# Performance work log

Hardware: AMD Instinct MI355X
Metric: run time of the kernel (lower is better)

The kernel has to match this reference:

```python
import jax, jax.numpy as jnp
import numpy as np

N = 100000          # nodes
E = 1_600_000       # edges (before self loops)
F_IN = 128          # node features
H = 4               # heads (gat1)
C = 32              # dim_h
HC = H * C
NC_CLONE = 20 - 1
NC_TYPE = 30 - 1
NEG_SLOPE = 0.2
BN_EPS = 1e-5


def setup_inputs() -> dict:
    key = jax.random.key(0)
    ks = jax.random.split(key, 24)
    rn = lambda k, shape, s=0.1: (jax.random.normal(k, shape, jnp.float32) * s)
    inp = {
        "x": jax.random.normal(ks[0], (N, F_IN), jnp.float32),
        "edge_index": jax.random.randint(ks[1], (2, E), 0, N, jnp.int32),
        "edge_attr": jax.random.uniform(ks[2], (E, 1), jnp.float32),
        # gat1 (GATv2Conv F_IN -> C, heads=H, edge_dim=1)
        "Wl1": rn(ks[3], (F_IN, HC)), "Wr1": rn(ks[4], (F_IN, HC)),
        "We1": rn(ks[5], (1, HC)), "att1": rn(ks[6], (H, C)), "b1": rn(ks[7], (HC,)),
        # skip Linear F_IN -> HC
        "skip_W": rn(ks[8], (F_IN, HC)), "skip_b": rn(ks[9], (HC,)),
        # batchnorm1
        "bn_g": jnp.ones((HC,), jnp.float32), "bn_b": jnp.zeros((HC,), jnp.float32),
        # gat2 (GATv2Conv HC -> C, heads=1, edge_dim=1)
        "Wl2": rn(ks[10], (HC, C)), "Wr2": rn(ks[11], (HC, C)),
        "We2": rn(ks[12], (1, C)), "att2": rn(ks[13], (1, C)), "b2": rn(ks[14], (C,)),
        # heads
        "fc1_W": rn(ks[15], (C, C)), "fc1_b": rn(ks[16], (C,)),
        "Wc": rn(ks[17], (C, NC_CLONE)), "bc": rn(ks[18], (NC_CLONE,)),
        "Wt": rn(ks[19], (C, NC_TYPE)), "bt": rn(ks[20], (NC_TYPE,)),
    }
    return inp


def _add_self_loops(src, dst, eattr, n):
    # PyG add_self_loops with fill_value='mean': loop attr = scatter-mean of edge_attr by dst
    deg = jax.ops.segment_sum(jnp.ones_like(eattr[:, 0]), dst, num_segments=n)
    mean_attr = jax.ops.segment_sum(eattr, dst, num_segments=n) / jnp.clip(deg, 1.0)[:, None]
    loop = jnp.arange(n, dtype=src.dtype)
    return (jnp.concatenate([src, loop]), jnp.concatenate([dst, loop]),
            jnp.concatenate([eattr, mean_attr], axis=0))


def _gatv2(x, src, dst, eattr, Wl, Wr, We, att, bias, heads, ch):
    n = x.shape[0]
    xl = (x @ Wl).reshape(n, heads, ch)   # values & source attention feats
    xr = (x @ Wr).reshape(n, heads, ch)   # target attention feats
    ee = (eattr @ We).reshape(-1, heads, ch)
    m = jax.nn.leaky_relu(xl[src] + xr[dst] + ee, NEG_SLOPE)   # [E,H,C]
    alpha = jnp.einsum('ehc,hc->eh', m, att)                   # [E,H]
    amax = jax.ops.segment_max(alpha, dst, num_segments=n)
    amax = jnp.where(jnp.isfinite(amax), amax, 0.0)
    ex = jnp.exp(alpha - amax[dst])
    den = jax.ops.segment_sum(ex, dst, num_segments=n)
    a = ex / (den[dst] + 1e-16)                                # segment softmax
    out = jax.ops.segment_sum(a[..., None] * xl[src], dst, num_segments=n)
    return out.reshape(n, heads * ch) + bias, a


def reference(x, edge_index, edge_attr, Wl1, Wr1, We1, att1, b1, skip_W, skip_b,
              bn_g, bn_b, Wl2, Wr2, We2, att2, b2, fc1_W, fc1_b, Wc, bc, Wt, bt):
    n = x.shape[0]
    src, dst, ea = _add_self_loops(edge_index[0], edge_index[1], edge_attr, n)
    h, _ = _gatv2(x, src, dst, ea, Wl1, Wr1, We1, att1, b1, H, C)
    h = h + x @ skip_W + skip_b
    mu = jnp.mean(h, axis=0)
    var = jnp.mean(jnp.square(h - mu), axis=0)
    h = (h - mu) * jax.lax.rsqrt(var + BN_EPS) * bn_g + bn_b
    h = jax.nn.elu(h)
    h, w = _gatv2(h, src, dst, ea, Wl2, Wr2, We2, att2, b2, 1, C)
    h = jax.nn.elu(h)
    h_last = jax.nn.relu(h @ fc1_W + fc1_b)
    h_type = jax.nn.log_softmax(h_last @ Wt + bt, axis=1)
    h_clone = jax.nn.log_softmax(h_last @ Wc + bc, axis=1)
    out = jnp.concatenate([h_clone, h_type], axis=1)
    return out, w
```

## Files before the change

### kernel.cpp

```cpp
#include <hip/hip_runtime.h>
#include <math.h>

#define NN 100000
#define EE 1600000
#define FIN 128
#define HCH 128
#define CCH 32
#define NCLONE 19
#define NTYPE 29
#define ETOT (EE + NN)
#define SCAN_B 49
#define LOG2E 1.4426950408889634f

typedef __bf16 bf16_t;
typedef bf16_t bf16x2 __attribute__((ext_vector_type(2)));
typedef bf16_t bf16x4 __attribute__((ext_vector_type(4)));
typedef bf16_t bf16x8 __attribute__((ext_vector_type(8)));
typedef float f32x4 __attribute__((ext_vector_type(4)));

__global__ __launch_bounds__(256) void k_wcvt(const float* __restrict__ Wl1,
                                              const float* __restrict__ Wr1,
                                              const float* __restrict__ Ws,
                                              const float* __restrict__ Wl2,
                                              const float* __restrict__ Wr2,
                                              bf16_t* __restrict__ WbT,
                                              bf16_t* __restrict__ Wb2T) {
    int t = blockIdx.x * 256 + threadIdx.x;
    if (t < 384 * 128) {
        int n = t >> 7, k = t & 127;
        const float* W = (n < 128) ? Wl1 : ((n < 256) ? Wr1 : Ws);
        WbT[t] = (bf16_t)W[k * 128 + (n & 127)];
    } else if (t < 384 * 128 + 64 * 128) {
        int u = t - 384 * 128;
        int n = u >> 7, k = u & 127;
        const float* W = (n < 32) ? Wl2 : Wr2;
        Wb2T[u] = (bf16_t)W[k * 32 + (n & 31)];
    }
}

__global__ __launch_bounds__(256) void k_deg(const int* __restrict__ ei,
                                             int* __restrict__ deg,
                                             int* __restrict__ slot) {
    int e = blockIdx.x * 256 + threadIdx.x;
    if (e < EE) {
        int d = ei[EE + e];
        slot[e] = atomicAdd(&deg[d], 1);
    }
}

__global__ __launch_bounds__(256) void k_scan1(const int* __restrict__ deg,
                                               int* __restrict__ offs,
                                               int* __restrict__ bsum) {
    __shared__ int tsum[256];
    int b = blockIdx.x, tid = threadIdx.x;
    int base = b * 2048;
    int loc[8];
    int s = 0;
    #pragma unroll
    for (int i = 0; i < 8; ++i) {
        int idx = base + tid * 8 + i;
        int d = (idx < NN) ? deg[idx] : 0;
        loc[i] = s; s += d;
    }
    tsum[tid] = s;
    __syncthreads();
    for (int off = 1; off < 256; off <<= 1) {
        int v = (tid >= off) ? tsum[tid - off] : 0;
        __syncthreads();
        tsum[tid] += v;
        __syncthreads();
    }
    int texcl = tsum[tid] - s;
    #pragma unroll
    for (int i = 0; i < 8; ++i) {
        int idx = base + tid * 8 + i;
        if (idx < NN) offs[idx] = texcl + loc[i];
    }
    if (tid == 255) bsum[b] = tsum[255];
}

__global__ void k_scan2(int* __restrict__ bsum) {
    if (threadIdx.x == 0) {
        int run = 0;
        for (int i = 0; i < SCAN_B; ++i) { int t = bsum[i]; bsum[i] = run; run += t; }
    }
}

__global__ __launch_bounds__(256) void k_scan3(int* __restrict__ offs,
                                               const int* __restrict__ bsum) {
    int i = blockIdx.x * 256 + threadIdx.x;
    if (i < NN) offs[i] += bsum[i >> 11];
}

__global__ __launch_bounds__(256) void k_fill(const int* __restrict__ ei,
                                              const float* __restrict__ ea,
                                              const int* __restrict__ offs,
                                              const int* __restrict__ slot,
                                              int2* __restrict__ ep8) {
    int e = blockIdx.x * 256 + threadIdx.x;
    if (e < EE) {
        int d = ei[EE + e];
        int pos = offs[d] + slot[e];
        ep8[pos] = make_int2(ei[e], __float_as_int(ea[e]));
    }
}

__global__ __launch_bounds__(256) void k_gemm1(const float* __restrict__ x,
                                               const bf16_t* __restrict__ WbT,
                                               bf16_t* __restrict__ xl,
                                               bf16_t* __restrict__ xr,
                                               bf16_t* __restrict__ sk) {
    __shared__ bf16_t As[128 * 128];
    __shared__ bf16_t Bs[128 * 128];
    const int tid = threadIdx.x;
    const int row0 = blockIdx.x * 128;
    #pragma unroll
    for (int i = 0; i < 8; ++i) {
        int c = i * 256 + tid;
        int r = c >> 4, g = c & 15;
        int gr = row0 + r;
        bf16x8 v = {};
        if (gr < NN) {
            float4 f0 = *(const float4*)(x + (size_t)gr * 128 + g * 8);
            float4 f1 = *(const float4*)(x + (size_t)gr * 128 + g * 8 + 4);
            v[0] = (bf16_t)f0.x; v[1] = (bf16_t)f0.y; v[2] = (bf16_t)f0.z; v[3] = (bf16_t)f0.w;
            v[4] = (bf16_t)f1.x; v[5] = (bf16_t)f1.y; v[6] = (bf16_t)f1.z; v[7] = (bf16_t)f1.w;
        }
        *(bf16x8*)&As[r * 128 + ((g ^ (r & 7)) * 8)] = v;
    }

    const int wid = tid >> 6, lane = tid & 63;
    const int wm = wid >> 1, wn = wid & 1;
    const int lr = lane & 15, lg = lane >> 4;

    for (int chunk = 0; chunk < 3; ++chunk) {
        const int col0 = chunk * 128;
        bf16_t* __restrict__ out = (chunk == 0) ? xl : ((chunk == 1) ? xr : sk);
        __syncthreads();
        #pragma unroll
        for (int i = 0; i < 8; ++i) {
            int c = i * 256 + tid;
            int n = c >> 4, g = c & 15;
            bf16x8 v = *(const bf16x8*)(WbT + (size_t)(col0 + n) * 128 + g * 8);
            *(bf16x8*)&Bs[n * 128 + ((g ^ (n & 7)) * 8)] = v;
        }
        __syncthreads();

        f32x4 acc[4][4] = {};
        #pragma unroll
        for (int ks = 0; ks < 4; ++ks) {
            int g = ks * 4 + lg;
            bf16x8 b[4];
            #pragma unroll
            for (int ni = 0; ni < 4; ++ni) {
                int n = wn * 64 + ni * 16 + lr;
                b[ni] = *(const bf16x8*)&Bs[n * 128 + ((g ^ (n & 7)) * 8)];
            }
            #pragma unroll
            for (int mi = 0; mi < 4; ++mi) {
                int r = wm * 64 + mi * 16 + lr;
                bf16x8 a = *(const bf16x8*)&As[r * 128 + ((g ^ (r & 7)) * 8)];
                #pragma unroll
                for (int ni = 0; ni < 4; ++ni)
                    acc[mi][ni] = __builtin_amdgcn_mfma_f32_16x16x32_bf16(a, b[ni], acc[mi][ni], 0, 0, 0);
            }
        }
        #pragma unroll
        for (int mi = 0; mi < 4; ++mi)
            #pragma unroll
            for (int ni = 0; ni < 4; ++ni)
                #pragma unroll
                for (int j = 0; j < 4; ++j) {
                    int gr = row0 + wm * 64 + mi * 16 + lg * 4 + j;
                    if (gr >= NN) continue;
                    int n = wn * 64 + ni * 16 + lr;
                    out[(size_t)gr * 128 + n] = (bf16_t)acc[mi][ni][j];
                }
    }
}

__global__ __launch_bounds__(256) void k_gat1(const bf16_t* __restrict__ xl1,
                                              const bf16_t* __restrict__ xr1,
                                              const bf16_t* __restrict__ skb,
                                              const int* __restrict__ offs,
                                              const int* __restrict__ deg,
                                              const int2* __restrict__ ep8,
                                              const float* __restrict__ att1,
                                              const float* __restrict__ we1,
                                              const float* __restrict__ b1,
                                              const float* __restrict__ skipb,
                                              bf16_t* __restrict__ hb,
                                              float* __restrict__ mattr) {
    int v = (blockIdx.x * 256 + threadIdx.x) >> 6;
    if (v >= NN) return;
    int lane = threadIdx.x & 63;
    int sub = lane >> 4;
    int l = lane & 15;
    int c0 = l * 8;
    float at[8], we[8], xr[8];
    {
        float4 t0 = *(const float4*)(att1 + c0);
        float4 t1 = *(const float4*)(att1 + c0 + 4);
        at[0] = t0.x * LOG2E; at[1] = t0.y * LOG2E; at[2] = t0.z * LOG2E; at[3] = t0.w * LOG2E;
        at[4] = t1.x * LOG2E; at[5] = t1.y * LOG2E; at[6] = t1.z * LOG2E; at[7] = t1.w * LOG2E;
        float4 w0 = *(const float4*)(we1 + c0);
        float4 w1 = *(const float4*)(we1 + c0 + 4);
        we[0] = w0.x; we[1] = w0.y; we[2] = w0.z; we[3] = w0.w;
        we[4] = w1.x; we[5] = w1.y; we[6] = w1.z; we[7] = w1.w;
        bf16x8 xrv = *(const bf16x8*)(xr1 + (size_t)v * 128 + c0);
        #pragma unroll
        for (int j = 0; j < 8; ++j) xr[j] = (float)xrv[j];
    }
    float den = 0.f, easum = 0.f;
    float n[8] = {};
    int st = offs[v], dg = deg[v];
    int i = sub;
    int2 e0 = make_int2(0, 0), e1 = make_int2(0, 0), e2 = make_int2(0, 0);
    bf16x8 a0 = {}, a1 = {};
    if (i < dg) e0 = ep8[st + i];
    if (i + 4 < dg) e1 = ep8[st + i + 4];
    if (i + 8 < dg) e2 = ep8[st + i + 8];
    if (i < dg) a0 = *(const bf16x8*)(xl1 + (size_t)e0.x * 128 + c0);
    if (i + 4 < dg) a1 = *(const bf16x8*)(xl1 + (size_t)e1.x * 128 + c0);
    for (; i < dg; i += 4) {
        bf16x8 a2 = {};
        int2 e3 = make_int2(0, 0);
        if (i + 8 < dg) a2 = *(const bf16x8*)(xl1 + (size_t)e2.x * 128 + c0);
        if (i + 12 < dg) e3 = ep8[st + i + 12];
        float ea_ = __int_as_float(e0.y);
        easum += ea_;
        float q = 0.f, xv[8];
        #pragma unroll
        for (int j = 0; j < 8; ++j) {
            xv[j] = (float)a0[j];
            float w_ = xv[j] + fmaf(ea_, we[j], xr[j]);
            w_ = (w_ > 0.f) ? w_ : 0.2f * w_;
            q = fmaf(w_, at[j], q);
        }
        q += __shfl_xor(q, 1, 4);
        q += __shfl_xor(q, 2, 4);
        float ex = exp2f(q);
        den += ex;
        #pragma unroll
        for (int j = 0; j < 8; ++j) n[j] = fmaf(ex, xv[j], n[j]);
        e0 = e1; e1 = e2; e2 = e3; a0 = a1; a1 = a2;
    }
    #pragma unroll
    for (int w_ = 16; w_ <= 32; w_ <<= 1) {
        den += __shfl_xor(den, w_, 64);
        easum += __shfl_xor(easum, w_, 64);
        #pragma unroll
        for (int j = 0; j < 8; ++j) n[j] += __shfl_xor(n[j], w_, 64);
    }
    float eav = easum / fmaxf((float)dg, 1.0f);
    if (lane == 0) mattr[v] = eav;
    bf16x8 svv = *(const bf16x8*)(xl1 + (size_t)v * 128 + c0);
    float qs = 0.f, xs[8];
    #pragma unroll
    for (int j = 0; j < 8; ++j) {
        xs[j] = (float)svv[j];
        float w_ = xs[j] + fmaf(eav, we[j], xr[j]);
        w_ = (w_ > 0.f) ? w_ : 0.2f * w_;
        qs = fmaf(w_, at[j], qs);
    }
    qs += __shfl_xor(qs, 1, 4);
    qs += __shfl_xor(qs, 2, 4);
    {
        float ex = exp2f(qs);
        den += ex;
        #pragma unroll
        for (int j = 0; j < 8; ++j) n[j] = fmaf(ex, xs[j], n[j]);
    }
    if (sub == 0) {
        float inv = 1.0f / (den + 1e-16f);
        float4 bb0 = *(const float4*)(b1 + c0);
        float4 bb1 = *(const float4*)(b1 + c0 + 4);
        float4 sb0 = *(const float4*)(skipb + c0);
        float4 sb1 = *(const float4*)(skipb + c0 + 4);
        bf16x8 skv = *(const bf16x8*)(skb + (size_t)v * 128 + c0);
        float bb[8] = {bb0.x, bb0.y, bb0.z, bb0.w, bb1.x, bb1.y, bb1.z, bb1.w};
        float sv[8] = {sb0.x, sb0.y, sb0.z, sb0.w, sb1.x, sb1.y, sb1.z, sb1.w};
        bf16x8 r;
        #pragma unroll
        for (int j = 0; j < 8; ++j)
            r[j] = (bf16_t)(n[j] * inv + bb[j] + (float)skv[j] + sv[j]);
        *(bf16x8*)(hb + (size_t)v * 128 + c0) = r;
    }
}

__global__ __launch_bounds__(256) void k_bnstats(const bf16_t* __restrict__ h,
                                                 float* __restrict__ bns,
                                                 float* __restrict__ bnq) {
    __shared__ float sS[16 * 128];
    __shared__ float sQ[16 * 128];
    int tid = threadIdx.x;
    int cg = tid & 15;
    int slot = tid >> 4;
    int c0 = cg * 8;
    float s[8] = {}, q[8] = {};
    for (int r = blockIdx.x * 16 + slot; r < NN; r += gridDim.x * 16) {
        bf16x8 v = *(const bf16x8*)&h[(size_t)r * 128 + c0];
        #pragma unroll
        for (int j = 0; j < 8; ++j) { float f = (float)v[j]; s[j] += f; q[j] += f * f; }
    }
    #pragma unroll
    for (int j = 0; j < 8; ++j) { sS[slot * 128 + c0 + j] = s[j]; sQ[slot * 128 + c0 + j] = q[j]; }
    __syncthreads();
    if (tid < 128) {
        float as = 0.f, aq = 0.f;
        #pragma unroll
        for (int k = 0; k < 16; ++k) { as += sS[k * 128 + tid]; aq += sQ[k * 128 + tid]; }
        atomicAdd(&bns[tid], as);
        atomicAdd(&bnq[tid], aq);
    }
}

__global__ void k_bnfinal(const float* __restrict__ bns, const float* __restrict__ bnq,
                          const float* __restrict__ g, const float* __restrict__ b,
                          float* __restrict__ scale, float* __restrict__ shift) {
    int c = threadIdx.x;
    if (c < 128) {
        float mu = bns[c] * (1.0f / NN);
        float var = bnq[c] * (1.0f / NN) - mu * mu;
        float rs = rsqrtf(var + 1e-5f);
        float a = rs * g[c];
        scale[c] = a;
        shift[c] = b[c] - mu * a;
    }
}

__global__ __launch_bounds__(256) void k_gemm2(const bf16_t* __restrict__ h,
                                               const float* __restrict__ scl,
                                               const float* __restrict__ shf,
                                               const bf16_t* __restrict__ Wb2T,
                                               bf16_t* __restrict__ xl2,
                                               float* __restrict__ xr2) {
    __shared__ bf16_t As[128 * 128];
    __shared__ bf16_t Bs[64 * 128];
    const int tid = threadIdx.x;
    const int row0 = blockIdx.x * 128;
    #pragma unroll
    for (int i = 0; i < 8; ++i) {
        int c = i * 256 + tid;
        int r = c >> 4, g = c & 15;
        int gr = row0 + r;
        bf16x8 v = {};
        if (gr < NN) {
            bf16x8 hv = *(const bf16x8*)(h + (size_t)gr * 128 + g * 8);
            float4 s0 = *(const float4*)(scl + g * 8);
            float4 s1 = *(const float4*)(scl + g * 8 + 4);
            float4 t0 = *(const float4*)(shf + g * 8);
            float4 t1 = *(const float4*)(shf + g * 8 + 4);
            float e[8];
            e[0] = (float)hv[0] * s0.x + t0.x; e[1] = (float)hv[1] * s0.y + t0.y;
            e[2] = (float)hv[2] * s0.z + t0.z; e[3] = (float)hv[3] * s0.w + t0.w;
            e[4] = (float)hv[4] * s1.x + t1.x; e[5] = (float)hv[5] * s1.y + t1.y;
            e[6] = (float)hv[6] * s1.z + t1.z; e[7] = (float)hv[7] * s1.w + t1.w;
            #pragma unroll
            for (int j = 0; j < 8; ++j) {
                float vv = e[j];
                vv = (vv > 0.f) ? vv : (__expf(vv) - 1.0f);
                v[j] = (bf16_t)vv;
            }
        }
        *(bf16x8*)&As[r * 128 + ((g ^ (r & 7)) * 8)] = v;
    }
    #pragma unroll
    for (int i = 0; i < 4; ++i) {
        int c = i * 256 + tid;
        int n = c >> 4, g = c & 15;
        bf16x8 v = *(const bf16x8*)(Wb2T + (size_t)n * 128 + g * 8);
        *(bf16x8*)&Bs[n * 128 + ((g ^ (n & 7)) * 8)] = v;
    }
    __syncthreads();

    const int wid = tid >> 6, lane = tid & 63;
    const int wm = wid >> 1, wn = wid & 1;
    const int lr = lane & 15, lg = lane >> 4;
    f32x4 acc[4][2] = {};
    #pragma unroll
    for (int ks = 0; ks < 4; ++ks) {
        int g = ks * 4 + lg;
        bf16x8 b0, b1;
        {
            int n = wn * 32 + lr;
            b0 = *(const bf16x8*)&Bs[n * 128 + ((g ^ (n & 7)) * 8)];
            n += 16;
            b1 = *(const bf16x8*)&Bs[n * 128 + ((g ^ (n & 7)) * 8)];
        }
        #pragma unroll
        for (int mi = 0; mi < 4; ++mi) {
            int r = wm * 64 + mi * 16 + lr;
            bf16x8 a = *(const bf16x8*)&As[r * 128 + ((g ^ (r & 7)) * 8)];
            acc[mi][0] = __builtin_amdgcn_mfma_f32_16x16x32_bf16(a, b0, acc[mi][0], 0, 0, 0);
            acc[mi][1] = __builtin_amdgcn_mfma_f32_16x16x32_bf16(a, b1, acc[mi][1], 0, 0, 0);
        }
    }
    #pragma unroll
    for (int mi = 0; mi < 4; ++mi)
        #pragma unroll
        for (int ni = 0; ni < 2; ++ni)
            #pragma unroll
            for (int j = 0; j < 4; ++j) {
                int gr = row0 + wm * 64 + mi * 16 + lg * 4 + j;
                if (gr >= NN) continue;
                int n = wn * 32 + ni * 16 + lr;
                float val = acc[mi][ni][j];
                if (n < 32) xl2[(size_t)gr * 32 + n] = (bf16_t)val;
                else xr2[(size_t)gr * 32 + (n - 32)] = val;
            }
}

__global__ __launch_bounds__(256) void k_gat2(const bf16_t* __restrict__ xl2,
                                              const float* __restrict__ xr2,
                                              const float* __restrict__ mattr,
                                              const int* __restrict__ offs,
                                              const int* __restrict__ deg,
                                              const int2* __restrict__ ep8,
                                              const float* __restrict__ att2,
                                              const float* __restrict__ we2,
                                              const float* __restrict__ b2,
                                              float* __restrict__ h3,
                                              float* __restrict__ acsr,
                                              float* __restrict__ Inv,
                                              float* __restrict__ wout) {
    int v = (blockIdx.x * 256 + threadIdx.x) >> 6;
    if (v >= NN) return;
    int lane = threadIdx.x & 63;
    int sub = lane >> 3;
    int l = lane & 7;
    int c0 = l * 4;
    float4 atv = *(const float4*)(att2 + c0);
    float4 wev = *(const float4*)(we2 + c0);
    float4 xrv = *(const float4*)(xr2 + (size_t)v * 32 + c0);
    float at[4] = {atv.x * LOG2E, atv.y * LOG2E, atv.z * LOG2E, atv.w * LOG2E};
    float we[4] = {wev.x, wev.y, wev.z, wev.w};
    float xr[4] = {xrv.x, xrv.y, xrv.z, xrv.w};
    float den = 0.f;
    float n[4] = {};
    int st = offs[v], dg = deg[v];
    int i = sub;
    int2 e0 = make_int2(0, 0), e1 = make_int2(0, 0), e2 = make_int2(0, 0);
    bf16x4 a0 = {}, a1 = {};
    if (i < dg) e0 = ep8[st + i];
    if (i + 8 < dg) e1 = ep8[st + i + 8];
    if (i + 16 < dg) e2 = ep8[st + i + 16];
    if (i < dg) a0 = *(const bf16x4*)(xl2 + (size_t)e0.x * 32 + c0);
    if (i + 8 < dg) a1 = *(const bf16x4*)(xl2 + (size_t)e1.x * 32 + c0);
    for (; i < dg; i += 8) {
        bf16x4 a2 = {};
        int2 e3 = make_int2(0, 0);
        if (i + 16 < dg) a2 = *(const bf16x4*)(xl2 + (size_t)e2.x * 32 + c0);
        if (i + 24 < dg) e3 = ep8[st + i + 24];
        float ea_ = __int_as_float(e0.y);
        float q = 0.f, xv[4];
        #pragma unroll
        for (int j = 0; j < 4; ++j) {
            xv[j] = (float)a0[j];
            float w_ = xv[j] + fmaf(ea_, we[j], xr[j]);
            w_ = (w_ > 0.f) ? w_ : 0.2f * w_;
            q = fmaf(w_, at[j], q);
        }
        q += __shfl_xor(q, 1, 8);
        q += __shfl_xor(q, 2, 8);
        q += __shfl_xor(q, 4, 8);
        if (l == 0) acsr[st + i] = q;
        float ex = exp2f(q);
        den += ex;
        #pragma unroll
        for (int j = 0; j < 4; ++j) n[j] = fmaf(ex, xv[j], n[j]);
        e0 = e1; e1 = e2; e2 = e3; a0 = a1; a1 = a2;
    }
    #pragma unroll
    for (int w_ = 8; w_ <= 32; w_ <<= 1) {
        den += __shfl_xor(den, w_, 64);
        #pragma unroll
        for (int j = 0; j < 4; ++j) n[j] += __shfl_xor(n[j], w_, 64);
    }
    float eav = mattr[v];
    bf16x4 sv = *(const bf16x4*)(xl2 + (size_t)v * 32 + c0);
    float qs = 0.f, xs[4];
    #pragma unroll
    for (int j = 0; j < 4; ++j) {
        xs[j] = (float)sv[j];
        float w_ = xs[j] + fmaf(eav, we[j], xr[j]);
        w_ = (w_ > 0.f) ? w_ : 0.2f * w_;
        qs = fmaf(w_, at[j], qs);
    }
    qs += __shfl_xor(qs, 1, 8);
    qs += __shfl_xor(qs, 2, 8);
    qs += __shfl_xor(qs, 4, 8);
    {
        float ex = exp2f(qs);
        den += ex;
        #pragma unroll
        for (int j = 0; j < 4; ++j) n[j] = fmaf(ex, xs[j], n[j]);
    }
    float inv = 1.0f / (den + 1e-16f);
    if (lane == 0) {
        Inv[v] = inv;
        wout[EE + v] = exp2f(qs) * inv;
    }
    if (sub == 0) {
        float4 bb = *(const float4*)(b2 + c0);
        float b_[4] = {bb.x, bb.y, bb.z, bb.w};
        float4 r;
        float* rp = &r.x;
        #pragma unroll
        for (int j = 0; j < 4; ++j) {
            float o = n[j] * inv + b_[j];
            rp[j] = (o > 0.f) ? o : (__expf(o) - 1.0f);
        }
        *(float4*)(h3 + (size_t)v * 32 + c0) = r;
    }
}

__global__ __launch_bounds__(256) void k_wfinal(const int* __restrict__ ei,
                                                const int* __restrict__ offs,
                                                const int* __restrict__ slot,
                                                const float* __restrict__ acsr,
                                                const float* __restrict__ Inv,
                                                float* __restrict__ wout) {
    int e = blockIdx.x * 256 + threadIdx.x;
    if (e >= EE) return;
    int d = ei[EE + e];
    float al = acsr[offs[d] + slot[e]];
    wout[e] = exp2f(al) * Inv[d];
}

__global__ __launch_bounds__(256) void k_head(const float* __restrict__ h3,
                                              const float* __restrict__ fc1W,
                                              const float* __restrict__ fc1b,
                                              const float* __restrict__ Wc,
                                              const float* __restrict__ bc,
                                              const float* __restrict__ Wt,
                                              const float* __restrict__ bt,
                                              float* __restrict__ outp) {
    __shared__ float sW1[32 * 32];
    __shared__ float sWc[32 * NCLONE];
    __shared__ float sWt[32 * NTYPE];
    __shared__ float sb1[32], sbc[NCLONE], sbt[NTYPE];
    int tid = threadIdx.x;
    for (int i = tid; i < 1024; i += 256) sW1[i] = fc1W[i];
    for (int i = tid; i < 32 * NCLONE; i += 256) sWc[i] = Wc[i];
    for (int i = tid; i < 32 * NTYPE; i += 256) sWt[i] = Wt[i];
    if (tid < 32) sb1[tid] = fc1b[tid];
    if (tid < NCLONE) sbc[tid] = bc[tid];
    if (tid < NTYPE) sbt[tid] = bt[tid];
    __syncthreads();
    int g = tid >> 5, l = tid & 31;
    int v = blockIdx.x * 8 + g;
    if (v >= NN) return;
    float x = h3[(size_t)v * CCH + l];
    float acc = sb1[l];
    #pragma unroll
    for (int c = 0; c < 32; ++c) {
        float xc = __shfl(x, c, 32);
        acc += xc * sW1[c * 32 + l];
    }
    float hl = fmaxf(acc, 0.0f);
    float at = (l < NTYPE) ? sbt[l] : 0.0f;
    float ac = (l < NCLONE) ? sbc[l] : 0.0f;
    #pragma unroll
    for (int c = 0; c < 32; ++c) {
        float hc = __shfl(hl, c, 32);
        float wt_ = (l < NTYPE) ? sWt[c * NTYPE + l] : 0.0f;
        float wc_ = (l < NCLONE) ? sWc[c * NCLONE + l] : 0.0f;
        at += hc * wt_;
        ac += hc * wc_;
    }
    float vt = (l < NTYPE) ? at : -INFINITY;
    float mt = vt;
    mt = fmaxf(mt, __shfl_xor(mt, 16, 32));
    mt = fmaxf(mt, __shfl_xor(mt, 8, 32));
    mt = fmaxf(mt, __shfl_xor(mt, 4, 32));
    mt = fmaxf(mt, __shfl_xor(mt, 2, 32));
    mt = fmaxf(mt, __shfl_xor(mt, 1, 32));
    float et = __expf(vt - mt);
    float stt = et;
    stt += __shfl_xor(stt, 16, 32);
    stt += __shfl_xor(stt, 8, 32);
    stt += __shfl_xor(stt, 4, 32);
    stt += __shfl_xor(stt, 2, 32);
    stt += __shfl_xor(stt, 1, 32);
    float lt = vt - mt - logf(stt);
    float vc = (l < NCLONE) ? ac : -INFINITY;
    float mc = vc;
    mc = fmaxf(mc, __shfl_xor(mc, 16, 32));
    mc = fmaxf(mc, __shfl_xor(mc, 8, 32));
    mc = fmaxf(mc, __shfl_xor(mc, 4, 32));
    mc = fmaxf(mc, __shfl_xor(mc, 2, 32));
    mc = fmaxf(mc, __shfl_xor(mc, 1, 32));
    float ec = __expf(vc - mc);
    float sc = ec;
    sc += __shfl_xor(sc, 16, 32);
    sc += __shfl_xor(sc, 8, 32);
    sc += __shfl_xor(sc, 4, 32);
    sc += __shfl_xor(sc, 2, 32);
    sc += __shfl_xor(sc, 1, 32);
    float lc = vc - mc - logf(sc);
    size_t ob = (size_t)v * 48;
    if (l < NCLONE) outp[ob + l] = lc;
    if (l < NTYPE) outp[ob + NCLONE + l] = lt;
}

extern "C" void kernel_launch(void* const* d_in, const int* in_sizes, int n_in,
                              void* d_out, int out_size, void* d_ws, size_t ws_size,
                              hipStream_t stream) {
    const float* x     = (const float*)d_in[0];
    const int*   ei    = (const int*)d_in[1];
    const float* ea    = (const float*)d_in[2];
    const float* Wl1   = (const float*)d_in[3];
    const float* Wr1   = (const float*)d_in[4];
    const float* We1   = (const float*)d_in[5];
    const float* att1  = (const float*)d_in[6];
    const float* b1    = (const float*)d_in[7];
    const float* skipW = (const float*)d_in[8];
    const float* skipb = (const float*)d_in[9];
    const float* bng   = (const float*)d_in[10];
    const float* bnb   = (const float*)d_in[11];
    const float* Wl2   = (const float*)d_in[12];
    const float* Wr2   = (const float*)d_in[13];
    const float* We2   = (const float*)d_in[14];
    const float* att2  = (const float*)d_in[15];
    const float* b2    = (const float*)d_in[16];
    const float* fc1W  = (const float*)d_in[17];
    const float* fc1b  = (const float*)d_in[18];
    const float* Wc    = (const float*)d_in[19];
    const float* bc    = (const float*)d_in[20];
    const float* Wt    = (const float*)d_in[21];
    const float* bt    = (const float*)d_in[22];
    float* out = (float*)d_out;
    float* wout = out + (size_t)NN * 48;

    const size_t NF = (size_t)NN * FIN;
    char* w = (char*)d_ws;
    bf16_t* xl1b = (bf16_t*)w;  w += NF * 2;
    bf16_t* xr1b = (bf16_t*)w;  w += NF * 2;
    bf16_t* skb  = (bf16_t*)w;  w += NF * 2;
    bf16_t* hb   = (bf16_t*)w;  w += NF * 2;
    int2*   ep8  = (int2*)w;    w += (size_t)EE * 8;
    float*  acsr = (float*)w;   w += (size_t)EE * 4;
    int*    slot = (int*)w;     w += (size_t)EE * 4;
    int* deg   = (int*)w;   w += (size_t)NN * 4;
    int* offs  = (int*)w;   w += (size_t)NN * 4;
    float* mattr = (float*)w; w += (size_t)NN * 4;
    float* Inv   = (float*)w; w += (size_t)NN * 4;
    int*   bsum  = (int*)w;   w += 64 * 4;
    float* bns   = (float*)w; w += 128 * 4;
    float* bnq   = (float*)w; w += 128 * 4;
    float* scl   = (float*)w; w += 128 * 4;
    float* shf   = (float*)w; w += 128 * 4;
    bf16_t* WbT  = (bf16_t*)w; w += 384 * 128 * 2;
    bf16_t* Wb2T = (bf16_t*)w; w += 64 * 128 * 2;
    bf16_t* xl2b = xl1b;
    float*  xr2  = (float*)xr1b;
    float*  h3   = (float*)skb;

    hipMemsetAsync(deg, 0, (size_t)NN * sizeof(int), stream);
    hipMemsetAsync(bns, 0, 256 * sizeof(float), stream);

    k_wcvt<<<224, 256, 0, stream>>>(Wl1, Wr1, skipW, Wl2, Wr2, WbT, Wb2T);

    k_deg<<<6250, 256, 0, stream>>>(ei, deg, slot);
    k_scan1<<<SCAN_B, 256, 0, stream>>>(deg, offs, bsum);
    k_scan2<<<1, 64, 0, stream>>>(bsum);
    k_scan3<<<391, 256, 0, stream>>>(offs, bsum);
    k_fill<<<6250, 256, 0, stream>>>(ei, ea, offs, slot, ep8);

    k_gemm1<<<782, 256, 0, stream>>>(x, WbT, xl1b, xr1b, skb);
    k_gat1<<<25000, 256, 0, stream>>>(xl1b, xr1b, skb, offs, deg, ep8,
                                      att1, We1, b1, skipb, hb, mattr);
    k_bnstats<<<128, 256, 0, stream>>>(hb, bns, bnq);
    k_bnfinal<<<1, 128, 0, stream>>>(bns, bnq, bng, bnb, scl, shf);
    k_gemm2<<<782, 256, 0, stream>>>(hb, scl, shf, Wb2T, xl2b, xr2);
    k_gat2<<<25000, 256, 0, stream>>>(xl2b, xr2, mattr, offs, deg, ep8,
                                      att2, We2, b2, h3, acsr, Inv, wout);
    k_wfinal<<<6250, 256, 0, stream>>>(ei, offs, slot, acsr, Inv, wout);
    k_head<<<12500, 256, 0, stream>>>(h3, fc1W, fc1b, Wc, bc, Wt, bt, out);
}
```

Baseline: 450.2 us.

## Schedule GAT nodes by degree-sorted permutation and split unguarded steady-state edge loop

Adds a histogram, bin scan and scatter pass that builds a node permutation ordered from high to low in-degree, and both GAT aggregation kernels now process nodes in that order. Waves in a block then handle nodes of similar degree, which is meant to cut load imbalance and idle lanes from the per-node edge loops. The edge loops are also split into an unguarded steady-state part and a guarded tail, and the LeakyReLU select becomes fmaxf. In exchange there are three extra small launches and an extra indirect load per node, and output writes become scattered rather than sequential in node order.

```diff
diff --git a/kernel.cpp b/kernel.cpp
--- a/kernel.cpp
+++ b/kernel.cpp
@@ -10,6 +10,7 @@
 #define NTYPE 29
 #define ETOT (EE + NN)
 #define SCAN_B 49
+#define NBIN 128
 #define LOG2E 1.4426950408889634f
 
 typedef __bf16 bf16_t;
@@ -48,6 +49,46 @@
     }
 }
 
+__global__ __launch_bounds__(256) void k_hist(const int* __restrict__ deg,
+                                              int* __restrict__ hist) {
+    __shared__ int lh[NBIN];
+    int tid = threadIdx.x;
+    if (tid < NBIN) lh[tid] = 0;
+    __syncthreads();
+    int v = blockIdx.x * 256 + tid;
+    if (v < NN) atomicAdd(&lh[min(deg[v], NBIN - 1)], 1);
+    __syncthreads();
+    if (tid < NBIN && lh[tid]) atomicAdd(&hist[tid], lh[tid]);
+}
+
+__global__ void k_bscan(const int* __restrict__ hist, int* __restrict__ binpos) {
+    if (threadIdx.x == 0) {
+        int run = 0;
+        for (int b = NBIN - 1; b >= 0; --b) { binpos[b] = run; run += hist[b]; }
+    }
+}
+
+__global__ __launch_bounds__(256) void k_scat(const int* __restrict__ deg,
+                                              int* __restrict__ binpos,
+                                              int* __restrict__ perm) {
+    __shared__ int lcnt[NBIN];
+    __shared__ int lbase[NBIN];
+    int tid = threadIdx.x;
+    if (tid < NBIN) lcnt[tid] = 0;
+    __syncthreads();
+    int v = blockIdx.x * 256 + tid;
+    int b = 0, r = 0;
+    bool ok = (v < NN);
+    if (ok) {
+        b = min(deg[v], NBIN - 1);
+        r = atomicAdd(&lcnt[b], 1);
+    }
+    __syncthreads();
+    if (tid < NBIN && lcnt[tid]) lbase[tid] = atomicAdd(&binpos[tid], lcnt[tid]);
+    __syncthreads();
+    if (ok) perm[lbase[b] + r] = v;
+}
+
 __global__ __launch_bounds__(256) void k_scan1(const int* __restrict__ deg,
                                                int* __restrict__ offs,
                                                int* __restrict__ bsum) {
@@ -179,7 +220,8 @@
     }
 }
 
-__global__ __launch_bounds__(256) void k_gat1(const bf16_t* __restrict__ xl1,
+__global__ __launch_bounds__(256) void k_gat1(const int* __restrict__ perm,
+                                              const bf16_t* __restrict__ xl1,
                                               const bf16_t* __restrict__ xr1,
                                               const bf16_t* __restrict__ skb,
                                               const int* __restrict__ offs,
@@ -191,8 +233,9 @@
                                               const float* __restrict__ skipb,
                                               bf16_t* __restrict__ hb,
                                               float* __restrict__ mattr) {
-    int v = (blockIdx.x * 256 + threadIdx.x) >> 6;
-    if (v >= NN) return;
+    int gid = (blockIdx.x * 256 + threadIdx.x) >> 6;
+    if (gid >= NN) return;
+    int v = perm[gid];
     int lane = threadIdx.x & 63;
     int sub = lane >> 4;
     int l = lane & 15;
@@ -222,29 +265,41 @@
     if (i + 8 < dg) e2 = ep8[st + i + 8];
     if (i < dg) a0 = *(const bf16x8*)(xl1 + (size_t)e0.x * 128 + c0);
     if (i + 4 < dg) a1 = *(const bf16x8*)(xl1 + (size_t)e1.x * 128 + c0);
+
+#define GAT1_BODY                                              \
+    {                                                          \
+        float ea_ = __int_as_float(e0.y);                      \
+        easum += ea_;                                          \
+        float q = 0.f, xv[8];                                  \
+        _Pragma("unroll")                                      \
+        for (int j = 0; j < 8; ++j) {                          \
+            xv[j] = (float)a0[j];                              \
+            float w_ = xv[j] + fmaf(ea_, we[j], xr[j]);        \
+            w_ = fmaxf(w_, 0.2f * w_);                         \
+            q = fmaf(w_, at[j], q);                            \
+        }                                                      \
+        q += __shfl_xor(q, 1, 4);                              \
+        q += __shfl_xor(q, 2, 4);                              \
+        float ex = exp2f(q);                                   \
+        den += ex;                                             \
+        _Pragma("unroll")                                      \
+        for (int j = 0; j < 8; ++j) n[j] = fmaf(ex, xv[j], n[j]); \
+        e0 = e1; e1 = e2; e2 = e3; a0 = a1; a1 = a2;           \
+    }
+
+    for (; i + 12 < dg; i += 4) {
+        bf16x8 a2 = *(const bf16x8*)(xl1 + (size_t)e2.x * 128 + c0);
+        int2 e3 = ep8[st + i + 12];
+        GAT1_BODY
+    }
     for (; i < dg; i += 4) {
         bf16x8 a2 = {};
         int2 e3 = make_int2(0, 0);
         if (i + 8 < dg) a2 = *(const bf16x8*)(xl1 + (size_t)e2.x * 128 + c0);
-        if (i + 12 < dg) e3 = ep8[st + i + 12];
-        float ea_ = __int_as_float(e0.y);
-        easum += ea_;
-        float q = 0.f, xv[8];
-        #pragma unroll
-        for (int j = 0; j < 8; ++j) {
-            xv[j] = (float)a0[j];
-            float w_ = xv[j] + fmaf(ea_, we[j], xr[j]);
-            w_ = (w_ > 0.f) ? w_ : 0.2f * w_;
-            q = fmaf(w_, at[j], q);
-        }
-        q += __shfl_xor(q, 1, 4);
-        q += __shfl_xor(q, 2, 4);
-        float ex = exp2f(q);
-        den += ex;
-        #pragma unroll
-        for (int j = 0; j < 8; ++j) n[j] = fmaf(ex, xv[j], n[j]);
-        e0 = e1; e1 = e2; e2 = e3; a0 = a1; a1 = a2;
-    }
+        GAT1_BODY
+    }
+#undef GAT1_BODY
+
     #pragma unroll
     for (int w_ = 16; w_ <= 32; w_ <<= 1) {
         den += __shfl_xor(den, w_, 64);
@@ -260,7 +315,7 @@
     for (int j = 0; j < 8; ++j) {
         xs[j] = (float)svv[j];
         float w_ = xs[j] + fmaf(eav, we[j], xr[j]);
-        w_ = (w_ > 0.f) ? w_ : 0.2f * w_;
+        w_ = fmaxf(w_, 0.2f * w_);
         qs = fmaf(w_, at[j], qs);
     }
     qs += __shfl_xor(qs, 1, 4);
@@ -411,7 +466,8 @@
             }
 }
 
-__global__ __launch_bounds__(256) void k_gat2(const bf16_t* __restrict__ xl2,
+__global__ __launch_bounds__(256) void k_gat2(const int* __restrict__ perm,
+                                              const bf16_t* __restrict__ xl2,
                                               const float* __restrict__ xr2,
                                               const float* __restrict__ mattr,
                                               const int* __restrict__ offs,
@@ -424,8 +480,9 @@
                                               float* __restrict__ acsr,
                                               float* __restrict__ Inv,
                                               float* __restrict__ wout) {
-    int v = (blockIdx.x * 256 + threadIdx.x) >> 6;
-    if (v >= NN) return;
+    int gid = (blockIdx.x * 256 + threadIdx.x) >> 6;
+    if (gid >= NN) return;
+    int v = perm[gid];
     int lane = threadIdx.x & 63;
     int sub = lane >> 3;
     int l = lane & 7;
@@ -447,30 +504,42 @@
     if (i + 16 < dg) e2 = ep8[st + i + 16];
     if (i < dg) a0 = *(const bf16x4*)(xl2 + (size_t)e0.x * 32 + c0);
     if (i + 8 < dg) a1 = *(const bf16x4*)(xl2 + (size_t)e1.x * 32 + c0);
+
+#define GAT2_BODY                                              \
+    {                                                          \
+        float ea_ = __int_as_float(e0.y);                      \
+        float q = 0.f, xv[4];                                  \
+        _Pragma("unroll")                                      \
+        for (int j = 0; j < 4; ++j) {                          \
+            xv[j] = (float)a0[j];                              \
+            float w_ = xv[j] + fmaf(ea_, we[j], xr[j]);        \
+            w_ = fmaxf(w_, 0.2f * w_);                         \
+            q = fmaf(w_, at[j], q);                            \
+        }                                                      \
+        q += __shfl_xor(q, 1, 8);                              \
+        q += __shfl_xor(q, 2, 8);                              \
+        q += __shfl_xor(q, 4, 8);                              \
+        if (l == 0) acsr[st + i] = q;                          \
+        float ex = exp2f(q);                                   \
+        den += ex;                                             \
+        _Pragma("unroll")                                      \
+        for (int j = 0; j < 4; ++j) n[j] = fmaf(ex, xv[j], n[j]); \
+        e0 = e1; e1 = e2; e2 = e3; a0 = a1; a1 = a2;           \
+    }
+
+    for (; i + 24 < dg; i += 8) {
+        bf16x4 a2 = *(const bf16x4*)(xl2 + (size_t)e2.x * 32 + c0);
+        int2 e3 = ep8[st + i + 24];
+        GAT2_BODY
+    }
     for (; i < dg; i += 8) {
         bf16x4 a2 = {};
         int2 e3 = make_int2(0, 0);
         if (i + 16 < dg) a2 = *(const bf16x4*)(xl2 + (size_t)e2.x * 32 + c0);
-        if (i + 24 < dg) e3 = ep8[st + i + 24];
-        float ea_ = __int_as_float(e0.y);
-        float q = 0.f, xv[4];
-        #pragma unroll
-        for (int j = 0; j < 4; ++j) {
-            xv[j] = (float)a0[j];
-            float w_ = xv[j] + fmaf(ea_, we[j], xr[j]);
-            w_ = (w_ > 0.f) ? w_ : 0.2f * w_;
-            q = fmaf(w_, at[j], q);
-        }
-        q += __shfl_xor(q, 1, 8);
-        q += __shfl_xor(q, 2, 8);
-        q += __shfl_xor(q, 4, 8);
-        if (l == 0) acsr[st + i] = q;
-        float ex = exp2f(q);
-        den += ex;
-        #pragma unroll
-        for (int j = 0; j < 4; ++j) n[j] = fmaf(ex, xv[j], n[j]);
-        e0 = e1; e1 = e2; e2 = e3; a0 = a1; a1 = a2;
-    }
+        GAT2_BODY
+    }
+#undef GAT2_BODY
+
     #pragma unroll
     for (int w_ = 8; w_ <= 32; w_ <<= 1) {
         den += __shfl_xor(den, w_, 64);
@@ -484,7 +553,7 @@
     for (int j = 0; j < 4; ++j) {
         xs[j] = (float)sv[j];
         float w_ = xs[j] + fmaf(eav, we[j], xr[j]);
-        w_ = (w_ > 0.f) ? w_ : 0.2f * w_;
+        w_ = fmaxf(w_, 0.2f * w_);
         qs = fmaf(w_, at[j], qs);
     }
     qs += __shfl_xor(qs, 1, 8);
@@ -646,9 +715,12 @@
     int* offs  = (int*)w;   w += (size_t)NN * 4;
     float* mattr = (float*)w; w += (size_t)NN * 4;
     float* Inv   = (float*)w; w += (size_t)NN * 4;
+    int*   perm  = (int*)w;   w += (size_t)NN * 4;
     int*   bsum  = (int*)w;   w += 64 * 4;
     float* bns   = (float*)w; w += 128 * 4;
     float* bnq   = (float*)w; w += 128 * 4;
+    int*   hist  = (int*)w;   w += NBIN * 4;
+    int*   binpos= (int*)w;   w += NBIN * 4;
     float* scl   = (float*)w; w += 128 * 4;
     float* shf   = (float*)w; w += 128 * 4;
     bf16_t* WbT  = (bf16_t*)w; w += 384 * 128 * 2;
@@ -658,23 +730,26 @@
     float*  h3   = (float*)skb;
 
     hipMemsetAsync(deg, 0, (size_t)NN * sizeof(int), stream);
-    hipMemsetAsync(bns, 0, 256 * sizeof(float), stream);
+    hipMemsetAsync(bns, 0, (256 + NBIN) * sizeof(float), stream);
 
     k_wcvt<<<224, 256, 0, stream>>>(Wl1, Wr1, skipW, Wl2, Wr2, WbT, Wb2T);
 
     k_deg<<<6250, 256, 0, stream>>>(ei, deg, slot);
+    k_hist<<<391, 256, 0, stream>>>(deg, hist);
+    k_bscan<<<1, 64, 0, stream>>>(hist, binpos);
+    k_scat<<<391, 256, 0, stream>>>(deg, binpos, perm);
     k_scan1<<<SCAN_B, 256, 0, stream>>>(deg, offs, bsum);
     k_scan2<<<1, 64, 0, stream>>>(bsum);
     k_scan3<<<391, 256, 0, stream>>>(offs, bsum);
     k_fill<<<6250, 256, 0, stream>>>(ei, ea, offs, slot, ep8);
 
     k_gemm1<<<782, 256, 0, stream>>>(x, WbT, xl1b, xr1b, skb);
-    k_gat1<<<25000, 256, 0, stream>>>(xl1b, xr1b, skb, offs, deg, ep8,
+    k_gat1<<<25000, 256, 0, stream>>>(perm, xl1b, xr1b, skb, offs, deg, ep8,
                                       att1, We1, b1, skipb, hb, mattr);
     k_bnstats<<<128, 256, 0, stream>>>(hb, bns, bnq);
     k_bnfinal<<<1, 128, 0, stream>>>(bns, bnq, bng, bnb, scl, shf);
     k_gemm2<<<782, 256, 0, stream>>>(hb, scl, shf, Wb2T, xl2b, xr2);
-    k_gat2<<<25000, 256, 0, stream>>>(xl2b, xr2, mattr, offs, deg, ep8,
+    k_gat2<<<25000, 256, 0, stream>>>(perm, xl2b, xr2, mattr, offs, deg, ep8,
                                       att2, We2, b2, h3, acsr, Inv, wout);
     k_wfinal<<<6250, 256, 0, stream>>>(ei, offs, slot, acsr, Inv, wout);
     k_head<<<12500, 256, 0, stream>>>(h3, fc1W, fc1b, Wc, bc, Wt, bt, out);
```

Measured after the change: 449.1 us. Within noise of the previous version (-0.2%).
